# Kernel tuning notes

Hardware: AMD Instinct MI355X
Metric: run time of the kernel (lower is better)

## Reference

```python
import jax, jax.numpy as jnp
import numpy as np

H = 128          # hidden_dim
B = 4096         # number of graphs (segments)
N = 1048576      # total nodes
NUM_OBS = 1


def setup_inputs() -> dict:
    key = jax.random.key(0)
    ks = jax.random.split(key, 10)
    h = jax.random.normal(ks[0], (N, H), dtype=jnp.float32)
    batch = jnp.sort(jax.random.randint(ks[1], (N,), 0, B, dtype=jnp.int64))
    s = 1.0 / np.sqrt(H)
    s2 = 1.0 / np.sqrt(2 * H)
    # gate: Linear(H,H) -> tanh -> Linear(H,1)
    gate_w1 = jax.random.uniform(ks[2], (H, H), jnp.float32, -s, s)
    gate_b1 = jax.random.uniform(ks[3], (H,), jnp.float32, -s, s)
    gate_w2 = jax.random.uniform(ks[4], (H, 1), jnp.float32, -s, s)
    gate_b2 = jax.random.uniform(ks[5], (1,), jnp.float32, -s, s)
    # mlp: Linear(2H,H) -> ReLU -> Linear(H,num_obs)  (dropout off in eval)
    mlp_w1 = jax.random.uniform(ks[6], (2 * H, H), jnp.float32, -s2, s2)
    mlp_b1 = jax.random.uniform(ks[7], (H,), jnp.float32, -s2, s2)
    mlp_w2 = jax.random.uniform(ks[8], (H, NUM_OBS), jnp.float32, -s, s)
    mlp_b2 = jax.random.uniform(ks[9], (NUM_OBS,), jnp.float32, -s, s)
    return {"h": h, "batch": batch,
            "gate_w1": gate_w1, "gate_b1": gate_b1,
            "gate_w2": gate_w2, "gate_b2": gate_b2,
            "mlp_w1": mlp_w1, "mlp_b1": mlp_b1,
            "mlp_w2": mlp_w2, "mlp_b2": mlp_b2}


def reference(h, batch, gate_w1, gate_b1, gate_w2, gate_b2,
              mlp_w1, mlp_b1, mlp_w2, mlp_b2):
    # gate scores per node: (N,)
    score = (jnp.tanh(h @ gate_w1 + gate_b1) @ gate_w2 + gate_b2)[:, 0]
    # segment softmax over nodes of each graph (numerically stable)
    seg_max = jax.ops.segment_max(score, batch, num_segments=B)
    e = jnp.exp(score - seg_max[batch])
    seg_sum = jax.ops.segment_sum(e, batch, num_segments=B)
    attn = e / seg_sum[batch]                      # (N,)
    # attention-weighted sum pooling: (B, H)
    g_attn = jax.ops.segment_sum(h * attn[:, None], batch, num_segments=B)
    # max pooling: (B, H)
    g_max = jax.ops.segment_max(h, batch, num_segments=B)
    g = jnp.concatenate([g_attn, g_max], axis=-1)  # (B, 2H)
    hidden = jax.nn.relu(g @ mlp_w1 + mlp_b1)
    return hidden @ mlp_w2 + mlp_b2               # (B, NUM_OBS)
```

## Files before the change

### kernel.cpp

```cpp
#include <hip/hip_runtime.h>
#include <hip/hip_bf16.h>
#include <cfloat>

#define HD 128

typedef float f32x4 __attribute__((ext_vector_type(4)));
typedef __bf16 bf16x8 __attribute__((ext_vector_type(8)));

__global__ void seg_bounds_kernel(const int* __restrict__ batch, int n, int nseg,
                                  int* __restrict__ seg_start) {
  int b = blockIdx.x * blockDim.x + threadIdx.x;
  if (b > nseg) return;
  if (b == nseg) { seg_start[b] = n; return; }
  int lo = 0, hi = n;
  while (lo < hi) {
    int mid = (lo + hi) >> 1;
    if (batch[mid] < b) lo = mid + 1; else hi = mid;
  }
  seg_start[b] = lo;
}


#define LOAD_TILE(BUF, T)                                                   \
  {                                                                         \
    const int nIt_ = (T) * 16 + lr;                                         \
    const size_t row_ = (size_t)s0 + (size_t)min(nIt_, len - 1);            \
    const float* hp_ = h + row_ * HD + 8 * kl;                              \
    _Pragma("unroll")                                                       \
    for (int kt = 0; kt < 4; ++kt) {                                        \
      *reinterpret_cast<float4*>(&BUF[8 * kt]) =                            \
          *reinterpret_cast<const float4*>(hp_ + 32 * kt);                  \
      *reinterpret_cast<float4*>(&BUF[8 * kt + 4]) =                        \
          *reinterpret_cast<const float4*>(hp_ + 32 * kt + 4);              \
    }                                                                       \
  }

#define PROC_TILE(BUF, T)                                                   \
  {                                                                         \
    const bool valid_ = ((T) * 16 + lr) < len;                              \
    bf16x8 a_[4];                                                           \
    _Pragma("unroll")                                                       \
    for (int kt = 0; kt < 4; ++kt)                                          \
      _Pragma("unroll")                                                     \
      for (int j = 0; j < 8; ++j) a_[kt][j] = (__bf16)BUF[8 * kt + j];      \
    int ob_ = 0;                                                            \
    asm volatile("" : "+v"(ob_));                                           \
    const __bf16* wp_ = sWt + ob_;                                          \
    f32x4 macc_[8];                                                         \
    _Pragma("unroll")                                                       \
    for (int f = 0; f < 8; ++f) macc_[f] = (f32x4){0.f, 0.f, 0.f, 0.f};     \
    _Pragma("unroll")                                                       \
    for (int kt = 0; kt < 4; ++kt) {                                        \
      _Pragma("unroll")                                                     \
      for (int f = 0; f < 8; ++f) {                                         \
        const int c_ = 16 * f + lr;                                         \
        const bf16x8 bfr_ = *reinterpret_cast<const bf16x8*>(               \
            wp_ + c_ * HD + (((4 * kt + kl) ^ (c_ & 15)) << 3));            \
        macc_[f] =                                                          \
            __builtin_amdgcn_mfma_f32_16x16x32_bf16(a_[kt], bfr_, macc_[f], \
                                                    0, 0, 0);               \
      }                                                                     \
    }                                                                       \
    float p2_[4] = {0.f, 0.f, 0.f, 0.f};                                    \
    _Pragma("unroll")                                                       \
    for (int f = 0; f < 8; ++f) {                                           \
      _Pragma("unroll")                                                     \
      for (int r = 0; r < 4; ++r) {                                         \
        const float xe_ = fmaf(LOG2E2, macc_[f][r], b1s[f]);                \
        const float e_ = exp2f(xe_);                                        \
        const float t_ = __builtin_amdgcn_rcpf(1.f + e_);                   \
        p2_[r] = fmaf(t_, w2r[f], p2_[r]);                                  \
      }                                                                     \
    }                                                                       \
    _Pragma("unroll")                                                       \
    for (int r = 0; r < 4; ++r) {                                           \
      p2_[r] += __shfl_xor(p2_[r], 1, 16);                                  \
      p2_[r] += __shfl_xor(p2_[r], 2, 16);                                  \
      p2_[r] += __shfl_xor(p2_[r], 4, 16);                                  \
      p2_[r] += __shfl_xor(p2_[r], 8, 16);                                  \
    }                                                                       \
    const float minp_ = fminf(fminf(p2_[0], p2_[1]), fminf(p2_[2], p2_[3]));\
    float tmax_ = fmaf(-2.f, minp_, sumW2);                                 \
    tmax_ = fmaxf(tmax_, __shfl_xor(tmax_, 16, 64));                        \
    tmax_ = fmaxf(tmax_, __shfl_xor(tmax_, 32, 64));                        \
    const int rr_ = lr & 3;                                                 \
    const float psel_ =                                                     \
        rr_ == 0 ? p2_[0] : (rr_ == 1 ? p2_[1] : (rr_ == 2 ? p2_[2]         \
                                                            : p2_[3]));     \
    const float vsc_ = fmaf(-2.f, psel_, sumW2);                            \
    const float sc_ = __shfl(vsc_, ((lr >> 2) << 4) | (lr & 3), 64);        \
    if (tmax_ > m) {                                                        \
      const float scl_ = exp2f((m - tmax_) * LOG2E);                        \
      s *= scl_;                                                            \
      _Pragma("unroll")                                                     \
      for (int j = 0; j < 32; ++j) acc[j] *= scl_;                          \
      m = tmax_;                                                            \
    }                                                                       \
    const float w_ = valid_ ? exp2f((sc_ - m) * LOG2E) : 0.f;               \
    s += w_;                                                                \
    _Pragma("unroll")                                                       \
    for (int j = 0; j < 32; ++j) {                                          \
      acc[j] = fmaf(BUF[j], w_, acc[j]);                                    \
      gm[j] = fmaxf(gm[j], BUF[j]);                                         \
    }                                                                       \
  }

__global__ __launch_bounds__(256, 2) void fused_pool_kernel(
    const float* __restrict__ h, const float* __restrict__ w1,
    const float* __restrict__ b1, const float* __restrict__ w2,
    const int* __restrict__ seg_start, float* __restrict__ g, int B)
{
  __shared__ __bf16 sWt[HD * HD];

  for (int i = threadIdx.x; i < HD * HD / 4; i += 256) {
    const int k = i >> 5;
    const int c4 = (i & 31) << 2;
    const float4 v = reinterpret_cast<const float4*>(w1)[i];
    const float vv[4] = {v.x, v.y, v.z, v.w};
#pragma unroll
    for (int q = 0; q < 4; ++q) {
      const int c = c4 + q;
      sWt[c * HD + ((((k >> 3) ^ (c & 15)) << 3) | (k & 7))] = (__bf16)vv[q];
    }
  }
  __syncthreads();

  const float LOG2E  = 1.44269504088896341f;
  const float LOG2E2 = 2.88539008177792681f;

  const int lane = threadIdx.x & 63;
  const int wid  = threadIdx.x >> 6;
  const int lr   = lane & 15;
  const int kl   = lane >> 4;

  float w2r[8], b1s[8];
#pragma unroll
  for (int f = 0; f < 8; ++f) {
    w2r[f] = w2[16 * f + lr];
    b1s[f] = LOG2E2 * b1[16 * f + lr];
  }
  float sumW2 = 0.f;
#pragma unroll
  for (int f = 0; f < 8; ++f) sumW2 += w2r[f];
  sumW2 += __shfl_xor(sumW2, 1, 16);
  sumW2 += __shfl_xor(sumW2, 2, 16);
  sumW2 += __shfl_xor(sumW2, 4, 16);
  sumW2 += __shfl_xor(sumW2, 8, 16);

  const int segStride = gridDim.x * 4;
  for (int b = blockIdx.x * 4 + wid; b < B; b += segStride) {
    const int s0  = seg_start[b];
    const int len = seg_start[b + 1] - s0;
    const int nt  = (len + 15) >> 4;

    float m = -FLT_MAX, s = 0.f;
    float acc[32], gm[32];
#pragma unroll
    for (int j = 0; j < 32; ++j) { acc[j] = 0.f; gm[j] = -FLT_MAX; }

    if (nt > 0) {
      float hA[32], hB[32];
      LOAD_TILE(hA, 0)
      int t = 0;
      for (; t + 1 < nt; t += 2) {
        LOAD_TILE(hB, t + 1)
        PROC_TILE(hA, t)
        if (t + 2 < nt) LOAD_TILE(hA, t + 2)
        PROC_TILE(hB, t + 1)
      }
      if (t < nt) PROC_TILE(hA, t)
    }

#pragma unroll
    for (int off = 1; off <= 8; off <<= 1) {
      s += __shfl_xor(s, off, 16);
#pragma unroll
      for (int j = 0; j < 32; ++j) {
        acc[j] += __shfl_xor(acc[j], off, 16);
        gm[j] = fmaxf(gm[j], __shfl_xor(gm[j], off, 16));
      }
    }

    if (lr == 0) {
      const float invS = (s > 0.f) ? 1.f / s : 0.f;
#pragma unroll
      for (int kt = 0; kt < 4; ++kt) {
        const int fb = 32 * kt + 8 * kl;
        float4 va, vb, ma, mb;
        va.x = acc[8*kt+0]*invS; va.y = acc[8*kt+1]*invS;
        va.z = acc[8*kt+2]*invS; va.w = acc[8*kt+3]*invS;
        vb.x = acc[8*kt+4]*invS; vb.y = acc[8*kt+5]*invS;
        vb.z = acc[8*kt+6]*invS; vb.w = acc[8*kt+7]*invS;
        ma.x = gm[8*kt+0]; ma.y = gm[8*kt+1]; ma.z = gm[8*kt+2]; ma.w = gm[8*kt+3];
        mb.x = gm[8*kt+4]; mb.y = gm[8*kt+5]; mb.z = gm[8*kt+6]; mb.w = gm[8*kt+7];
        *reinterpret_cast<float4*>(&g[(size_t)b * 256 + fb])       = va;
        *reinterpret_cast<float4*>(&g[(size_t)b * 256 + fb + 4])   = vb;
        *reinterpret_cast<float4*>(&g[(size_t)b * 256 + 128 + fb]) = ma;
        *reinterpret_cast<float4*>(&g[(size_t)b * 256 + 128 + fb + 4]) = mb;
      }
    }
  }
}

__global__ __launch_bounds__(512) void mlp_kernel(
    const float* __restrict__ g, const float* __restrict__ w1,
    const float* __restrict__ b1, const float* __restrict__ w2,
    const float* __restrict__ b2, float* __restrict__ out)
{
  __shared__ float sg[4][256];
  __shared__ float sred[4][2];
  const int t = threadIdx.x;
  const int sidx = t >> 7;
  const int u = t & 127;
  const int b0 = blockIdx.x * 4;
  sg[sidx][u]       = g[(size_t)(b0 + sidx) * 256 + u];
  sg[sidx][u + 128] = g[(size_t)(b0 + sidx) * 256 + 128 + u];
  __syncthreads();
  float acc = b1[u];
#pragma unroll 8
  for (int k = 0; k < 256; ++k)
    acc = fmaf(sg[sidx][k], w1[k * HD + u], acc);
  float v = fmaxf(acc, 0.f) * w2[u];
#pragma unroll
  for (int off = 32; off >= 1; off >>= 1) v += __shfl_xor(v, off, 64);
  if ((t & 63) == 0) sred[sidx][(t >> 6) & 1] = v;
  __syncthreads();
  if (u == 0) out[b0 + sidx] = sred[sidx][0] + sred[sidx][1] + b2[0];
}

extern "C" void kernel_launch(void* const* d_in, const int* in_sizes, int n_in,
                              void* d_out, int out_size, void* d_ws, size_t ws_size,
                              hipStream_t stream) {
  const float* h       = (const float*)d_in[0];
  const int*   batch   = (const int*)d_in[1];
  const float* gate_w1 = (const float*)d_in[2];
  const float* gate_b1 = (const float*)d_in[3];
  const float* gate_w2 = (const float*)d_in[4];
  const float* mlp_w1  = (const float*)d_in[6];
  const float* mlp_b1  = (const float*)d_in[7];
  const float* mlp_w2  = (const float*)d_in[8];
  const float* mlp_b2  = (const float*)d_in[9];
  float* out = (float*)d_out;

  const int N = in_sizes[0] / HD;
  const int B = out_size;

  char* ws = (char*)d_ws;
  float* g   = (float*)ws;
  int*   seg = (int*)(ws + (size_t)B * 256 * 4);

  seg_bounds_kernel<<<(B + 256) / 256, 256, 0, stream>>>(batch, N, B, seg);
  fused_pool_kernel<<<1024, 256, 0, stream>>>(h, gate_w1, gate_b1, gate_w2,
                                              seg, g, B);
  mlp_kernel<<<B / 4, 512, 0, stream>>>(g, mlp_w1, mlp_b1, mlp_w2, mlp_b2, out);
}
```

Baseline: 182.7 us.

## Use atomic work-stealing over segments, triple-buffer tile loads, precompute LDS offsets

Each wave now takes its next segment from a global atomic counter instead of a fixed grid-stride assignment, which balances segments of uneven length across waves. The counter is reset inside the bounds kernel. The tile loop becomes triple-buffered with an unconditional clamped prefetch, the swizzled LDS offsets for the weight fragments are computed once per wave, and the grid is halved to 512 blocks. The extra live buffer raises register pressure, the atomics add some contention, and the tail iterations process tiles that are masked out.

```diff
diff --git a/kernel.cpp b/kernel.cpp
--- a/kernel.cpp
+++ b/kernel.cpp
@@ -8,8 +8,9 @@
 typedef __bf16 bf16x8 __attribute__((ext_vector_type(8)));
 
 __global__ void seg_bounds_kernel(const int* __restrict__ batch, int n, int nseg,
-                                  int* __restrict__ seg_start) {
+                                  int* __restrict__ seg_start, int* __restrict__ ctr) {
   int b = blockIdx.x * blockDim.x + threadIdx.x;
+  if (b == 0) *ctr = 0;
   if (b > nseg) return;
   if (b == nseg) { seg_start[b] = n; return; }
   int lo = 0, hi = n;
@@ -24,7 +25,7 @@
 #define LOAD_TILE(BUF, T)                                                   \
   {                                                                         \
     const int nIt_ = (T) * 16 + lr;                                         \
-    const size_t row_ = (size_t)s0 + (size_t)min(nIt_, len - 1);            \
+    const size_t row_ = (size_t)s0 + (size_t)min(nIt_, lenm1);              \
     const float* hp_ = h + row_ * HD + 8 * kl;                              \
     _Pragma("unroll")                                                       \
     for (int kt = 0; kt < 4; ++kt) {                                        \
@@ -43,19 +44,19 @@
     for (int kt = 0; kt < 4; ++kt)                                          \
       _Pragma("unroll")                                                     \
       for (int j = 0; j < 8; ++j) a_[kt][j] = (__bf16)BUF[8 * kt + j];      \
-    int ob_ = 0;                                                            \
-    asm volatile("" : "+v"(ob_));                                           \
-    const __bf16* wp_ = sWt + ob_;                                          \
+                 \
+    asm volatile("" : "+v"(dsb[0]), "+v"(dsb[1]), "+v"(dsb[2]),             \
+                      "+v"(dsb[3]));                                        \
     f32x4 macc_[8];                                                         \
     _Pragma("unroll")                                                       \
     for (int f = 0; f < 8; ++f) macc_[f] = (f32x4){0.f, 0.f, 0.f, 0.f};     \
     _Pragma("unroll")                                                       \
     for (int kt = 0; kt < 4; ++kt) {                                        \
+      const char* bp_ = reinterpret_cast<const char*>(sWt) + dsb[kt];       \
       _Pragma("unroll")                                                     \
       for (int f = 0; f < 8; ++f) {                                         \
-        const int c_ = 16 * f + lr;                                         \
-        const bf16x8 bfr_ = *reinterpret_cast<const bf16x8*>(               \
-            wp_ + c_ * HD + (((4 * kt + kl) ^ (c_ & 15)) << 3));            \
+        const bf16x8 bfr_ =                                                 \
+            *reinterpret_cast<const bf16x8*>(bp_ + f * 4096);               \
         macc_[f] =                                                          \
             __builtin_amdgcn_mfma_f32_16x16x32_bf16(a_[kt], bfr_, macc_[f], \
                                                     0, 0, 0);               \
@@ -108,7 +109,8 @@
 __global__ __launch_bounds__(256, 2) void fused_pool_kernel(
     const float* __restrict__ h, const float* __restrict__ w1,
     const float* __restrict__ b1, const float* __restrict__ w2,
-    const int* __restrict__ seg_start, float* __restrict__ g, int B)
+    const int* __restrict__ seg_start, float* __restrict__ g, int B,
+    int* __restrict__ ctr)
 {
   __shared__ __bf16 sWt[HD * HD];
 
@@ -129,7 +131,6 @@
   const float LOG2E2 = 2.88539008177792681f;
 
   const int lane = threadIdx.x & 63;
-  const int wid  = threadIdx.x >> 6;
   const int lr   = lane & 15;
   const int kl   = lane >> 4;
 
@@ -147,10 +148,20 @@
   sumW2 += __shfl_xor(sumW2, 4, 16);
   sumW2 += __shfl_xor(sumW2, 8, 16);
 
-  const int segStride = gridDim.x * 4;
-  for (int b = blockIdx.x * 4 + wid; b < B; b += segStride) {
+  int dsb[4];
+#pragma unroll
+  for (int kt = 0; kt < 4; ++kt)
+    dsb[kt] = lr * 256 + (((4 * kt + kl) ^ lr) << 4);
+
+  for (;;) {
+    int b;
+    if (lane == 0) b = atomicAdd(ctr, 1);
+    b = __shfl(b, 0, 64);
+    if (b >= B) break;
+
     const int s0  = seg_start[b];
     const int len = seg_start[b + 1] - s0;
+    const int lenm1 = len - 1;
     const int nt  = (len + 15) >> 4;
 
     float m = -FLT_MAX, s = 0.f;
@@ -158,17 +169,16 @@
 #pragma unroll
     for (int j = 0; j < 32; ++j) { acc[j] = 0.f; gm[j] = -FLT_MAX; }
 
-    if (nt > 0) {
-      float hA[32], hB[32];
-      LOAD_TILE(hA, 0)
-      int t = 0;
-      for (; t + 1 < nt; t += 2) {
-        LOAD_TILE(hB, t + 1)
-        PROC_TILE(hA, t)
-        if (t + 2 < nt) LOAD_TILE(hA, t + 2)
-        PROC_TILE(hB, t + 1)
-      }
-      if (t < nt) PROC_TILE(hA, t)
+    float hA[32], hB[32], hC[32];
+    LOAD_TILE(hA, 0)
+    LOAD_TILE(hB, 1)
+    for (int t = 0; t < nt; t += 3) {
+      LOAD_TILE(hC, t + 2)
+      PROC_TILE(hA, t)
+      LOAD_TILE(hA, t + 3)
+      PROC_TILE(hB, t + 1)
+      LOAD_TILE(hB, t + 4)
+      PROC_TILE(hC, t + 2)
     }
 
 #pragma unroll
@@ -193,9 +203,9 @@
         vb.z = acc[8*kt+6]*invS; vb.w = acc[8*kt+7]*invS;
         ma.x = gm[8*kt+0]; ma.y = gm[8*kt+1]; ma.z = gm[8*kt+2]; ma.w = gm[8*kt+3];
         mb.x = gm[8*kt+4]; mb.y = gm[8*kt+5]; mb.z = gm[8*kt+6]; mb.w = gm[8*kt+7];
-        *reinterpret_cast<float4*>(&g[(size_t)b * 256 + fb])       = va;
-        *reinterpret_cast<float4*>(&g[(size_t)b * 256 + fb + 4])   = vb;
-        *reinterpret_cast<float4*>(&g[(size_t)b * 256 + 128 + fb]) = ma;
+        *reinterpret_cast<float4*>(&g[(size_t)b * 256 + fb])           = va;
+        *reinterpret_cast<float4*>(&g[(size_t)b * 256 + fb + 4])       = vb;
+        *reinterpret_cast<float4*>(&g[(size_t)b * 256 + 128 + fb])     = ma;
         *reinterpret_cast<float4*>(&g[(size_t)b * 256 + 128 + fb + 4]) = mb;
       }
     }
@@ -248,9 +258,10 @@
   char* ws = (char*)d_ws;
   float* g   = (float*)ws;
   int*   seg = (int*)(ws + (size_t)B * 256 * 4);
-
-  seg_bounds_kernel<<<(B + 256) / 256, 256, 0, stream>>>(batch, N, B, seg);
-  fused_pool_kernel<<<1024, 256, 0, stream>>>(h, gate_w1, gate_b1, gate_w2,
-                                              seg, g, B);
+  int*   ctr = seg + (B + 2);
+
+  seg_bounds_kernel<<<(B + 256) / 256, 256, 0, stream>>>(batch, N, B, seg, ctr);
+  fused_pool_kernel<<<512, 256, 0, stream>>>(h, gate_w1, gate_b1, gate_w2,
+                                             seg, g, B, ctr);
   mlp_kernel<<<B / 4, 512, 0, stream>>>(g, mlp_w1, mlp_b1, mlp_w2, mlp_b2, out);
 }
```

Result: slower. 333.0 us (+82.3%).

## Drop online softmax max tracking and precompute swizzled LDS weight addresses

Applied to the files above, without the earlier changes.

Scores come from a tanh-bounded gate, so the softmax uses the fixed shift sumW2. Each node weight becomes exp2(-2*log2e*p2), with p2 the accumulated gate partial. This removes the per-tile max reduction shuffles, the running-max rescale branch and the 32-element accumulator rescale. The W1 fragment addresses in LDS are now built from a precomputed per-lane byte offset, and all eight B fragments are loaded before the MFMAs are issued. The fixed shift stays safe only while the sum of |w2| is small enough that exp cannot overflow, so numerical safety now depends on the gate weight magnitudes.

```diff
diff --git a/kernel.cpp b/kernel.cpp
--- a/kernel.cpp
+++ b/kernel.cpp
@@ -24,7 +24,7 @@
 #define LOAD_TILE(BUF, T)                                                   \
   {                                                                         \
     const int nIt_ = (T) * 16 + lr;                                         \
-    const size_t row_ = (size_t)s0 + (size_t)min(nIt_, len - 1);            \
+    const size_t row_ = (size_t)s0 + (size_t)min(nIt_, lenm1);              \
     const float* hp_ = h + row_ * HD + 8 * kl;                              \
     _Pragma("unroll")                                                       \
     for (int kt = 0; kt < 4; ++kt) {                                        \
@@ -43,23 +43,24 @@
     for (int kt = 0; kt < 4; ++kt)                                          \
       _Pragma("unroll")                                                     \
       for (int j = 0; j < 8; ++j) a_[kt][j] = (__bf16)BUF[8 * kt + j];      \
-    int ob_ = 0;                                                            \
-    asm volatile("" : "+v"(ob_));                                           \
-    const __bf16* wp_ = sWt + ob_;                                          \
+                 \
+    asm volatile("" : "+v"(Cb));                                            \
     f32x4 macc_[8];                                                         \
     _Pragma("unroll")                                                       \
     for (int f = 0; f < 8; ++f) macc_[f] = (f32x4){0.f, 0.f, 0.f, 0.f};     \
     _Pragma("unroll")                                                       \
     for (int kt = 0; kt < 4; ++kt) {                                        \
-      _Pragma("unroll")                                                     \
-      for (int f = 0; f < 8; ++f) {                                         \
-        const int c_ = 16 * f + lr;                                         \
-        const bf16x8 bfr_ = *reinterpret_cast<const bf16x8*>(               \
-            wp_ + c_ * HD + (((4 * kt + kl) ^ (c_ & 15)) << 3));            \
+      const char* bp_ = reinterpret_cast<const char*>(sWt) +                \
+                        (Cb + ((kt ^ hi2) << 6));                           \
+      bf16x8 bfr_[8];                                                       \
+      _Pragma("unroll")                                                     \
+      for (int f = 0; f < 8; ++f)                                           \
+        bfr_[f] = *reinterpret_cast<const bf16x8*>(bp_ + f * 4096);         \
+      _Pragma("unroll")                                                     \
+      for (int f = 0; f < 8; ++f)                                           \
         macc_[f] =                                                          \
-            __builtin_amdgcn_mfma_f32_16x16x32_bf16(a_[kt], bfr_, macc_[f], \
-                                                    0, 0, 0);               \
-      }                                                                     \
+            __builtin_amdgcn_mfma_f32_16x16x32_bf16(a_[kt], bfr_[f],        \
+                                                    macc_[f], 0, 0, 0);     \
     }                                                                       \
     float p2_[4] = {0.f, 0.f, 0.f, 0.f};                                    \
     _Pragma("unroll")                                                       \
@@ -79,24 +80,12 @@
       p2_[r] += __shfl_xor(p2_[r], 4, 16);                                  \
       p2_[r] += __shfl_xor(p2_[r], 8, 16);                                  \
     }                                                                       \
-    const float minp_ = fminf(fminf(p2_[0], p2_[1]), fminf(p2_[2], p2_[3]));\
-    float tmax_ = fmaf(-2.f, minp_, sumW2);                                 \
-    tmax_ = fmaxf(tmax_, __shfl_xor(tmax_, 16, 64));                        \
-    tmax_ = fmaxf(tmax_, __shfl_xor(tmax_, 32, 64));                        \
     const int rr_ = lr & 3;                                                 \
     const float psel_ =                                                     \
         rr_ == 0 ? p2_[0] : (rr_ == 1 ? p2_[1] : (rr_ == 2 ? p2_[2]         \
                                                             : p2_[3]));     \
-    const float vsc_ = fmaf(-2.f, psel_, sumW2);                            \
-    const float sc_ = __shfl(vsc_, ((lr >> 2) << 4) | (lr & 3), 64);        \
-    if (tmax_ > m) {                                                        \
-      const float scl_ = exp2f((m - tmax_) * LOG2E);                        \
-      s *= scl_;                                                            \
-      _Pragma("unroll")                                                     \
-      for (int j = 0; j < 32; ++j) acc[j] *= scl_;                          \
-      m = tmax_;                                                            \
-    }                                                                       \
-    const float w_ = valid_ ? exp2f((sc_ - m) * LOG2E) : 0.f;               \
+    const float sc_ = __shfl(psel_, ((lr >> 2) << 4) | (lr & 3), 64);       \
+    const float w_ = valid_ ? exp2f(sc_ * NEG2LOG2E) : 0.f;                 \
     s += w_;                                                                \
     _Pragma("unroll")                                                       \
     for (int j = 0; j < 32; ++j) {                                          \
@@ -125,8 +114,8 @@
   }
   __syncthreads();
 
-  const float LOG2E  = 1.44269504088896341f;
-  const float LOG2E2 = 2.88539008177792681f;
+  const float LOG2E2    = 2.88539008177792681f;
+  const float NEG2LOG2E = -2.88539008177792681f;
 
   const int lane = threadIdx.x & 63;
   const int wid  = threadIdx.x >> 6;
@@ -139,21 +128,18 @@
     w2r[f] = w2[16 * f + lr];
     b1s[f] = LOG2E2 * b1[16 * f + lr];
   }
-  float sumW2 = 0.f;
-#pragma unroll
-  for (int f = 0; f < 8; ++f) sumW2 += w2r[f];
-  sumW2 += __shfl_xor(sumW2, 1, 16);
-  sumW2 += __shfl_xor(sumW2, 2, 16);
-  sumW2 += __shfl_xor(sumW2, 4, 16);
-  sumW2 += __shfl_xor(sumW2, 8, 16);
+
+  const int hi2 = (lr >> 2) & 3;
+  int Cb = lr * 256 + ((kl ^ (lr & 3)) << 4);
 
   const int segStride = gridDim.x * 4;
   for (int b = blockIdx.x * 4 + wid; b < B; b += segStride) {
     const int s0  = seg_start[b];
     const int len = seg_start[b + 1] - s0;
+    const int lenm1 = len - 1;
     const int nt  = (len + 15) >> 4;
 
-    float m = -FLT_MAX, s = 0.f;
+    float s = 0.f;
     float acc[32], gm[32];
 #pragma unroll
     for (int j = 0; j < 32; ++j) { acc[j] = 0.f; gm[j] = -FLT_MAX; }
@@ -193,9 +179,9 @@
         vb.z = acc[8*kt+6]*invS; vb.w = acc[8*kt+7]*invS;
         ma.x = gm[8*kt+0]; ma.y = gm[8*kt+1]; ma.z = gm[8*kt+2]; ma.w = gm[8*kt+3];
         mb.x = gm[8*kt+4]; mb.y = gm[8*kt+5]; mb.z = gm[8*kt+6]; mb.w = gm[8*kt+7];
-        *reinterpret_cast<float4*>(&g[(size_t)b * 256 + fb])       = va;
-        *reinterpret_cast<float4*>(&g[(size_t)b * 256 + fb + 4])   = vb;
-        *reinterpret_cast<float4*>(&g[(size_t)b * 256 + 128 + fb]) = ma;
+        *reinterpret_cast<float4*>(&g[(size_t)b * 256 + fb])           = va;
+        *reinterpret_cast<float4*>(&g[(size_t)b * 256 + fb + 4])       = vb;
+        *reinterpret_cast<float4*>(&g[(size_t)b * 256 + 128 + fb])     = ma;
         *reinterpret_cast<float4*>(&g[(size_t)b * 256 + 128 + fb + 4]) = mb;
       }
     }
```

Result: no change. 185.4 us (+1.5%).
